# Kernel tuning notes

Hardware: AMD Instinct MI355X
Metric: run time of the kernel (lower is better)

Reference implementation:

```python
import jax, jax.numpy as jnp
import numpy as np

H = 16       # num_heads
D = 128      # head dim (TokenShift requires D in {16,32,64,128})
BASE = 10000.0


def _shift_linear(x, W, Ws):
    # ShiftLinear: linear -> (B,T,H,D), then token_shift mixing current token
    # with previous token using data-dependent per-head weights.
    B, T, _ = x.shape
    y = (x @ W.T).reshape(B, T, H, D)
    p = jax.nn.sigmoid(x @ Ws.T)                      # (B,T,H) prev-token weight
    y_prev = jnp.pad(y, ((0, 0), (1, 0), (0, 0), (0, 0)))[:, :T]  # shift right by 1
    return y * (1.0 - p)[..., None] + y_prev * p[..., None]


def _rope(q, k):
    # Non-interleaved half-rotation, signs exactly as in the torch source:
    # y1 = x1*cos + x2*sin ; y2 = -x1*sin + x2*cos
    T = q.shape[1]
    half = D // 2
    inv = 1.0 / (BASE ** (jnp.arange(0, D, 2, dtype=jnp.float32) / D))  # (half,)
    freqs = jnp.outer(jnp.arange(T, dtype=jnp.float32), inv)            # (T,half)
    cos = jnp.cos(freqs)[None, :, None, :]
    sin = jnp.sin(freqs)[None, :, None, :]
    def rot(x):
        x1, x2 = x[..., :half], x[..., half:]
        return jnp.concatenate([x1 * cos + x2 * sin, -x1 * sin + x2 * cos], axis=-1)
    return rot(q), rot(k)


def setup_inputs() -> dict:
    key = jax.random.key(0)
    ks = jax.random.split(key, 10)
    B, T, C = 2, 2048, 2048
    s = 0.02
    return {
        "x":   jax.random.normal(ks[0], (B, T, C), jnp.float32),
        "Wq":  s * jax.random.normal(ks[1], (C, C), jnp.float32),
        "Wsq": s * jax.random.normal(ks[2], (H, C), jnp.float32),
        "Wk":  s * jax.random.normal(ks[3], (C, C), jnp.float32),
        "Wsk": s * jax.random.normal(ks[4], (H, C), jnp.float32),
        "Wv":  s * jax.random.normal(ks[5], (C, C), jnp.float32),
        "Wsv": s * jax.random.normal(ks[6], (H, C), jnp.float32),
        "Wf":  s * jax.random.normal(ks[7], (H, C), jnp.float32),
        "bf":  s * jax.random.normal(ks[8], (H,), jnp.float32),
        "Wo":  s * jax.random.normal(ks[9], (C, C), jnp.float32),
    }


def reference(x, Wq, Wsq, Wk, Wsk, Wv, Wsv, Wf, bf, Wo):
    B, T, C = x.shape
    q = _shift_linear(x, Wq, Wsq)          # (B,T,H,D)
    k = _shift_linear(x, Wk, Wsk)
    v = _shift_linear(x, Wv, Wsv)
    q, k = _rope(q, k)

    # forget gate: log f_t per head, cumulative log-decay
    logf = jax.nn.log_sigmoid(x @ Wf.T + bf)       # (B,T,H)
    cum = jnp.cumsum(logf, axis=1).transpose(0, 2, 1)  # (B,H,T)

    s = jnp.einsum('bthd,bshd->bhts', q, k) / np.sqrt(D).astype(np.float32)
    # decay bias D_ij = sum_{l=j+1}^{i} log f_l = cum_i - cum_j
    s = s + cum[:, :, :, None] - cum[:, :, None, :]
    causal = jnp.tril(jnp.ones((T, T), dtype=bool))
    s = jnp.where(causal[None, None], s, -jnp.inf)
    p = jax.nn.softmax(s, axis=-1)                 # (B,H,T,T)

    o = jnp.einsum('bhts,bshd->bthd', p, v).reshape(B, T, C)
    return o @ Wo.T
```

## Files before the change

kernel.cpp:

```cpp
#include <hip/hip_runtime.h>
#include <math.h>


typedef __attribute__((ext_vector_type(8))) short  shortx8;
typedef __attribute__((ext_vector_type(4))) float  floatx4;

#define DEV __device__ __forceinline__

DEV unsigned short f2bf(float f) {
    unsigned int u = __builtin_bit_cast(unsigned int, f);
    u += 0x7FFFu + ((u >> 16) & 1u);
    return (unsigned short)(u >> 16);
}
DEV float bf2f(unsigned short s) {
    unsigned int u = ((unsigned int)s) << 16;
    return __builtin_bit_cast(float, u);
}
DEV void async16(void* lds, const void* g) {
    __builtin_amdgcn_global_load_lds(
        (const __attribute__((address_space(1))) unsigned int*)g,
        (__attribute__((address_space(3))) unsigned int*)lds, 16, 0, 0);
}

__global__ void cvt_bf16(const float* __restrict__ in, unsigned short* __restrict__ out, int n8) {
    int i = blockIdx.x * 256 + threadIdx.x;
    if (i >= n8) return;
    float4 u = ((const float4*)in)[2 * i];
    float4 v = ((const float4*)in)[2 * i + 1];
    shortx8 r;
    r[0] = (short)f2bf(u.x); r[1] = (short)f2bf(u.y); r[2] = (short)f2bf(u.z); r[3] = (short)f2bf(u.w);
    r[4] = (short)f2bf(v.x); r[5] = (short)f2bf(v.y); r[6] = (short)f2bf(v.z); r[7] = (short)f2bf(v.w);
    *(shortx8*)(out + (size_t)i * 8) = r;
}

__global__ void rope_tab(float2* __restrict__ tab, float* __restrict__ kmaxp) {
    int i = blockIdx.x * 256 + threadIdx.x;
    if (i < 32) kmaxp[i] = 0.f;
    int d = i & 63, t = i >> 6;
    float inv = exp2f(-(float)d * (13.287712379549449f / 64.f));
    float sv, cv;
    sincosf((float)t * inv, &sv, &cv);
    tab[i] = make_float2(cv, sv);
}

__global__ void build_wcat(const float* __restrict__ Wsq, const float* __restrict__ Wsk,
                           const float* __restrict__ Wsv, const float* __restrict__ Wf,
                           unsigned short* __restrict__ out) {
    int i = blockIdx.x * 256 + threadIdx.x;
    int c8 = i & 255;
    int row = i >> 8;
    const float* src = nullptr;
    if      (row < 16) src = Wsq + (size_t)row * 2048;
    else if (row < 32) src = Wsk + (size_t)(row - 16) * 2048;
    else if (row < 48) src = Wsv + (size_t)(row - 32) * 2048;
    else if (row < 64) src = Wf  + (size_t)(row - 48) * 2048;
    shortx8 r = (shortx8){0,0,0,0,0,0,0,0};
    if (src) {
#pragma unroll
        for (int q = 0; q < 8; ++q) r[q] = (short)f2bf(src[c8 * 8 + q]);
    }
    *(shortx8*)(out + (size_t)i * 8) = r;
}

template <typename OutT>
__global__ __launch_bounds__(256)
void gemm_bt(const unsigned short* __restrict__ A, const unsigned short* __restrict__ B,
             OutT* __restrict__ C, int M, int N, int K) {
    __shared__ __align__(16) unsigned short As[2][128 * 32];
    __shared__ __align__(16) unsigned short Bs[2][128 * 32];
    const int tid  = threadIdx.x;
    const int lane = tid & 63;
    const int w    = tid >> 6;
    const int nwg  = gridDim.x * gridDim.y;
    const int bid0 = blockIdx.y * gridDim.x + blockIdx.x;
    const int bids = (bid0 & 7) * (nwg >> 3) + (bid0 >> 3);
    const int m0   = (bids % gridDim.x) * 128;
    const int n0   = (bids / gridDim.x) * 128;
    const int wr   = (w >> 1) * 64;
    const int wc   = (w & 1) * 64;
    const int l15  = lane & 15, lg = lane >> 4;
    const int nk   = K >> 5;
    const int c0   = w * 64 + lane;

    floatx4 acc[4][4];
#pragma unroll
    for (int i = 0; i < 4; ++i)
#pragma unroll
        for (int j = 0; j < 4; ++j) acc[i][j] = (floatx4){0.f, 0.f, 0.f, 0.f};

#pragma unroll
    for (int t = 0; t < 2; ++t) {
        int c = t * 256 + c0;
        int row = c >> 2, seg = c & 3;
        async16(&As[0][(t * 256 + w * 64) * 8], A + (size_t)(m0 + row) * K + seg * 8);
        async16(&Bs[0][(t * 256 + w * 64) * 8], B + (size_t)(n0 + row) * K + seg * 8);
    }
    int cur = 0;
    for (int kt = 0; kt < nk; ++kt) {
        __syncthreads();
        if (kt + 1 < nk) {
#pragma unroll
            for (int t = 0; t < 2; ++t) {
                int c = t * 256 + c0;
                int row = c >> 2, seg = c & 3;
                async16(&As[cur ^ 1][(t * 256 + w * 64) * 8],
                        A + (size_t)(m0 + row) * K + (kt + 1) * 32 + seg * 8);
                async16(&Bs[cur ^ 1][(t * 256 + w * 64) * 8],
                        B + (size_t)(n0 + row) * K + (kt + 1) * 32 + seg * 8);
            }
        }
        shortx8 af[4], bfr[4];
#pragma unroll
        for (int i = 0; i < 4; ++i) {
            af[i]  = *(const shortx8*)&As[cur][(wr + i * 16 + l15) * 32 + 8 * lg];
            bfr[i] = *(const shortx8*)&Bs[cur][(wc + i * 16 + l15) * 32 + 8 * lg];
        }
#pragma unroll
        for (int i = 0; i < 4; ++i)
#pragma unroll
            for (int j = 0; j < 4; ++j)
                acc[i][j] = __builtin_amdgcn_mfma_f32_16x16x32_bf16(af[i], bfr[j], acc[i][j], 0, 0, 0);
        cur ^= 1;
    }
#pragma unroll
    for (int i = 0; i < 4; ++i)
#pragma unroll
        for (int j = 0; j < 4; ++j)
#pragma unroll
            for (int r = 0; r < 4; ++r) {
                int row = m0 + wr + i * 16 + 4 * lg + r;
                int col = n0 + wc + j * 16 + l15;
                float v = acc[i][j][r];
                if constexpr (sizeof(OutT) == 2) C[(size_t)row * N + col] = (OutT)f2bf(v);
                else                             C[(size_t)row * N + col] = v;
            }
}

__global__ void cumsum_logf(const float* __restrict__ glog, const float* __restrict__ bfv,
                            float* __restrict__ cum) {
    __shared__ float sums[256];
    const int bh = blockIdx.x, b = bh >> 4, h = bh & 15;
    const int tid = threadIdx.x;
    const float bias = bfv[h];
    float v[8];
    float s = 0.f;
#pragma unroll
    for (int i = 0; i < 8; ++i) {
        int t = tid * 8 + i;
        float z = glog[(size_t)(b * 2048 + t) * 128 + 48 + h] + bias;
        float lf = (z >= 0.f) ? -log1pf(__expf(-z)) : (z - log1pf(__expf(z)));
        s += lf;
        v[i] = s;
    }
    sums[tid] = s;
    __syncthreads();
    for (int off = 1; off < 256; off <<= 1) {
        float t = (tid >= off) ? sums[tid - off] : 0.f;
        __syncthreads();
        sums[tid] += t;
        __syncthreads();
    }
    float basep = sums[tid] - s;
#pragma unroll
    for (int i = 0; i < 8; ++i)
        cum[(size_t)bh * 2048 + tid * 8 + i] = basep + v[i];
}

template <bool ROPE>
__global__ void shift_rope(const unsigned short* __restrict__ Y, int ldY, int yoff,
                           const float* __restrict__ glog, int gcol,
                           const float4* __restrict__ tab4, float* __restrict__ kmaxp,
                           unsigned short* __restrict__ Out) {
    int gid = blockIdx.x * 256 + threadIdx.x;
    int j = gid & 7;
    int h = (gid >> 3) & 15;
    int t = (gid >> 7) & 2047;
    int b = gid >> 18;
    const unsigned short* yp = Y + (size_t)(b * 2048 + t) * ldY + yoff + h * 128;
    float z  = glog[(size_t)(b * 2048 + t) * 128 + gcol + h];
    float pg = 1.f / (1.f + __expf(-z));
    shortx8 a1 = *(const shortx8*)(yp + j * 8);
    shortx8 a2 = *(const shortx8*)(yp + 64 + j * 8);
    shortx8 b1 = (shortx8){0,0,0,0,0,0,0,0}, b2 = b1;
    if (t > 0) {
        b1 = *(const shortx8*)(yp - ldY + j * 8);
        b2 = *(const shortx8*)(yp - ldY + 64 + j * 8);
    }
    float c_[8], s_[8];
    if (ROPE && tab4) {
        const float4* tp = tab4 + (size_t)t * 32 + j * 4;
#pragma unroll
        for (int k = 0; k < 4; ++k) {
            float4 v4 = tp[k];
            c_[2 * k] = v4.x; s_[2 * k] = v4.y;
            c_[2 * k + 1] = v4.z; s_[2 * k + 1] = v4.w;
        }
    }
    shortx8 o1, o2;
    float n2 = 0.f;
    const float kf = 13.287712379549449f / 64.f;
#pragma unroll
    for (int i = 0; i < 8; ++i) {
        float m1 = bf2f((unsigned short)a1[i]) * (1.f - pg) + bf2f((unsigned short)b1[i]) * pg;
        float m2 = bf2f((unsigned short)a2[i]) * (1.f - pg) + bf2f((unsigned short)b2[i]) * pg;
        n2 += m1 * m1 + m2 * m2;
        float r1, r2;
        if (ROPE) {
            float sv, cv;
            if (tab4) { cv = c_[i]; sv = s_[i]; }
            else {
                int d = j * 8 + i;
                float inv = exp2f(-(float)d * kf);
                sincosf((float)t * inv, &sv, &cv);
            }
            r1 =  m1 * cv + m2 * sv;
            r2 = -m1 * sv + m2 * cv;
        } else { r1 = m1; r2 = m2; }
        o1[i] = (short)f2bf(r1);
        o2[i] = (short)f2bf(r2);
    }
    if (kmaxp) {
        n2 += __shfl_xor(n2, 1);
        n2 += __shfl_xor(n2, 2);
        n2 += __shfl_xor(n2, 4);
        if (j == 0)
            atomicMax((int*)(kmaxp + (b * 16 + h)), __float_as_int(n2));
    }
    unsigned short* op = Out + (size_t)((b * 16 + h) * 2048 + t) * 128;
    *(shortx8*)(op + j * 8)      = o1;
    *(shortx8*)(op + 64 + j * 8) = o2;
}

__global__ void transpose_v(const unsigned short* __restrict__ V, unsigned short* __restrict__ Vt) {
    __shared__ unsigned short tile[32][33];
    const int bh = blockIdx.z;
    const int t0 = blockIdx.x * 32, d0 = blockIdx.y * 32;
    const int tx = threadIdx.x, ty = threadIdx.y;
#pragma unroll
    for (int i = 0; i < 4; ++i) {
        int row = ty + i * 8;
        tile[row][tx] = V[(size_t)(bh * 2048 + t0 + row) * 128 + d0 + tx];
    }
    __syncthreads();
#pragma unroll
    for (int i = 0; i < 4; ++i) {
        int drow = ty + i * 8;
        Vt[(size_t)(bh * 128 + d0 + drow) * 2048 + t0 + tx] = tile[tx][drow];
    }
}

__global__ __launch_bounds__(512)
void flash_fwd(const unsigned short* __restrict__ Q, const unsigned short* __restrict__ Km,
               const unsigned short* __restrict__ Vt, const float* __restrict__ cum,
               const float* __restrict__ kmaxp, unsigned short* __restrict__ O) {
    __shared__ __align__(16) unsigned short Ks[3][32 * 128];
    __shared__ __align__(16) unsigned short Vs[3][64 * 64];
    __shared__ __align__(16) float          cumLds[2048];
    __shared__ __align__(16) unsigned short Plds[8][16][40];
    __shared__ int wmin[8];
    const int tid = threadIdx.x, lane = tid & 63, w = tid >> 6;
    const int l15 = lane & 15, lg = lane >> 4;
    const int bh = blockIdx.y, b = bh >> 4, h = bh & 15;
    const int qx = blockIdx.x;
    const int q0 = qx * 128;
    const int qr = q0 + w * 16;
    const size_t base = (size_t)bh * (2048 * 128);
    const float isd = 0.08838834764831845f;
    const int ntiles = 4 * qx + 4;
    const int myn0 = ((qr + 15) >> 5) + 1;
    const int myn = myn0 < ntiles ? myn0 : ntiles;

    const int ik = w * 64 + lane;
    const int kr = ik >> 4, kc = ik & 15;
    const unsigned short* ksrc = Km + base + (size_t)kr * 128 + ((kc ^ (kr & 7)) * 8);
    const int vr = ik >> 3, vc = ik & 7;
    const int vcc = vc ^ (vr & 7);
    const unsigned short* vsrc = Vt + (size_t)(bh * 128 + 2 * vr + (vcc >> 2)) * 2048 + (vcc & 3) * 8;

    const int kx = l15 & 7;
    const int vconst = ((l15 >> 1) * 64) + ((((l15 & 1) * 4 + lg) ^ ((l15 >> 1) & 7)) * 8);

    async16(&cumLds[ik * 4], cum + (size_t)bh * 2048 + ik * 4);
    shortx8 aq[4];
#pragma unroll
    for (int kk = 0; kk < 4; ++kk)
        aq[kk] = *(const shortx8*)(Q + base + (size_t)(qr + l15) * 128 + kk * 32 + 8 * lg);
    float kn2 = kmaxp ? kmaxp[bh] : 0.f;
    asm volatile("s_waitcnt vmcnt(0)" ::: "memory");
    __syncthreads();

    float cum_t[4];
#pragma unroll
    for (int r = 0; r < 4; ++r) cum_t[r] = cumLds[qr + 4 * lg + r];

    int wstart = 0;
    if (kmaxp) {
        float qp = 0.f;
#pragma unroll
        for (int kk = 0; kk < 4; ++kk)
#pragma unroll
            for (int i = 0; i < 8; ++i) {
                float v = bf2f((unsigned short)aq[kk][i]);
                qp += v * v;
            }
        qp += __shfl_xor(qp, 16);
        qp += __shfl_xor(qp, 32);
        float qn2 = qp;
        qn2 = fmaxf(qn2, __shfl_xor(qn2, 1));
        qn2 = fmaxf(qn2, __shfl_xor(qn2, 2));
        qn2 = fmaxf(qn2, __shfl_xor(qn2, 4));
        qn2 = fmaxf(qn2, __shfl_xor(qn2, 8));
        float qkb = sqrtf(qn2 * kn2) * isd;
        float thr = cumLds[qr] + 2.f * qkb + 30.f;
        int lo = 0, hi = myn - 1;
        while (lo < hi) {
            int mid = (lo + hi) >> 1;
            if (cumLds[32 * mid + 31] > thr) lo = mid + 1; else hi = mid;
        }
        wstart = lo;
    }
    if (lane == 0) wmin[w] = wstart;
    __syncthreads();
    int s0b = wmin[0];
#pragma unroll
    for (int i = 1; i < 8; ++i) s0b = min(s0b, wmin[i]);

    const int t2 = (s0b + 1 < ntiles) ? s0b + 1 : s0b;
    async16(&Ks[0][ik * 8], ksrc + (size_t)s0b * 32 * 128);
    async16(&Vs[0][ik * 8], vsrc + s0b * 32);
    async16(&Ks[1][ik * 8], ksrc + (size_t)t2 * 32 * 128);
    async16(&Vs[1][ik * 8], vsrc + t2 * 32);

    floatx4 oacc[8];
#pragma unroll
    for (int d = 0; d < 8; ++d) oacc[d] = (floatx4){0.f, 0.f, 0.f, 0.f};
    float m[4]  = {-1e30f, -1e30f, -1e30f, -1e30f};
    float ls[4] = {0.f, 0.f, 0.f, 0.f};

    int bc = 0, bi = 2;
    for (int kt = s0b; kt < ntiles; ++kt) {
        if (kt + 1 < ntiles) { asm volatile("s_waitcnt vmcnt(2)" ::: "memory"); }
        else                 { asm volatile("s_waitcnt vmcnt(0)" ::: "memory"); }
        __builtin_amdgcn_s_barrier();
        if (kt + 2 < ntiles) {
            async16(&Ks[bi][ik * 8], ksrc + (size_t)(kt + 2) * 32 * 128);
            async16(&Vs[bi][ik * 8], vsrc + (kt + 2) * 32);
        }
        if (kt >= wstart && kt < myn) {
            const int s0 = kt * 32;
            floatx4 sacc[2];
            sacc[0] = (floatx4){0.f, 0.f, 0.f, 0.f};
            sacc[1] = (floatx4){0.f, 0.f, 0.f, 0.f};
#pragma unroll
            for (int sf = 0; sf < 2; ++sf)
#pragma unroll
                for (int kk = 0; kk < 4; ++kk) {
                    shortx8 bk = *(const shortx8*)&Ks[bc][(sf * 16 + l15) * 128 + (((kk * 4 + lg) ^ kx) * 8)];
                    sacc[sf] = __builtin_amdgcn_mfma_f32_16x16x32_bf16(aq[kk], bk, sacc[sf], 0, 0, 0);
                }
            float cs[2];
#pragma unroll
            for (int sf = 0; sf < 2; ++sf) cs[sf] = cumLds[s0 + sf * 16 + l15];

            float p[2][4];
            float tmax[4] = {-1e30f, -1e30f, -1e30f, -1e30f};
            const bool maskt = (s0 + 31 > qr);
#pragma unroll
            for (int sf = 0; sf < 2; ++sf)
#pragma unroll
                for (int r = 0; r < 4; ++r) {
                    float sv = sacc[sf][r] * isd + cum_t[r] - cs[sf];
                    if (maskt) {
                        int trow = qr + 4 * lg + r;
                        int scol = s0 + sf * 16 + l15;
                        if (scol > trow) sv = -1e30f;
                    }
                    p[sf][r] = sv;
                    tmax[r] = fmaxf(tmax[r], sv);
                }
#pragma unroll
            for (int r = 0; r < 4; ++r) {
                tmax[r] = fmaxf(tmax[r], __shfl_xor(tmax[r], 1));
                tmax[r] = fmaxf(tmax[r], __shfl_xor(tmax[r], 2));
                tmax[r] = fmaxf(tmax[r], __shfl_xor(tmax[r], 4));
                tmax[r] = fmaxf(tmax[r], __shfl_xor(tmax[r], 8));
            }
            float g = tmax[0] - m[0];
            g = fmaxf(g, tmax[1] - m[1]);
            g = fmaxf(g, tmax[2] - m[2]);
            g = fmaxf(g, tmax[3] - m[3]);
            if (!__all(g <= 8.0f)) {
                float scl[4];
#pragma unroll
                for (int r = 0; r < 4; ++r) {
                    float mn = fmaxf(m[r], tmax[r]);
                    scl[r] = __expf(m[r] - mn);
                    m[r] = mn;
                    ls[r] *= scl[r];
                }
#pragma unroll
                for (int d = 0; d < 8; ++d)
#pragma unroll
                    for (int r = 0; r < 4; ++r) oacc[d][r] *= scl[r];
            }
            float rs[4] = {0.f, 0.f, 0.f, 0.f};
#pragma unroll
            for (int sf = 0; sf < 2; ++sf)
#pragma unroll
                for (int r = 0; r < 4; ++r) {
                    float e = __expf(p[sf][r] - m[r]);
                    p[sf][r] = e;
                    rs[r] += e;
                }
#pragma unroll
            for (int r = 0; r < 4; ++r) {
                rs[r] += __shfl_xor(rs[r], 1);
                rs[r] += __shfl_xor(rs[r], 2);
                rs[r] += __shfl_xor(rs[r], 4);
                rs[r] += __shfl_xor(rs[r], 8);
                ls[r] += rs[r];
            }
#pragma unroll
            for (int sf = 0; sf < 2; ++sf)
#pragma unroll
                for (int r = 0; r < 4; ++r)
                    Plds[w][4 * lg + r][sf * 16 + l15] = f2bf(p[sf][r]);
            shortx8 pa = *(const shortx8*)&Plds[w][l15][8 * lg];
#pragma unroll
            for (int d = 0; d < 8; ++d) {
                shortx8 bv = *(const shortx8*)&Vs[bc][d * 512 + vconst];
                oacc[d] = __builtin_amdgcn_mfma_f32_16x16x32_bf16(pa, bv, oacc[d], 0, 0, 0);
            }
        }
        bc = (bc == 2) ? 0 : bc + 1;
        bi = (bi == 2) ? 0 : bi + 1;
    }
#pragma unroll
    for (int r = 0; r < 4; ++r) {
        float inv = 1.f / ls[r];
        int trow = qr + 4 * lg + r;
        size_t ob = (size_t)(b * 2048 + trow) * 2048 + h * 128;
#pragma unroll
        for (int d = 0; d < 8; ++d)
            O[ob + d * 16 + l15] = f2bf(oacc[d][r] * inv);
    }
}

extern "C" void kernel_launch(void* const* d_in, const int* in_sizes, int n_in,
                              void* d_out, int out_size, void* d_ws, size_t ws_size,
                              hipStream_t stream) {
    const float* x   = (const float*)d_in[0];
    const float* Wq  = (const float*)d_in[1];
    const float* Wsq = (const float*)d_in[2];
    const float* Wk  = (const float*)d_in[3];
    const float* Wsk = (const float*)d_in[4];
    const float* Wv  = (const float*)d_in[5];
    const float* Wsv = (const float*)d_in[6];
    const float* Wf  = (const float*)d_in[7];
    const float* bfv = (const float*)d_in[8];
    const float* Wo  = (const float*)d_in[9];
    float* out = (float*)d_out;
    char* ws = (char*)d_ws;

    if (ws_size >= 146538880ull) {
        unsigned short* xb    = (unsigned short*)(ws + 0);
        unsigned short* Wb3   = (unsigned short*)(ws + 16777216);
        unsigned short* wcat  = (unsigned short*)(ws + 41943040);
        float*          glog  = (float*)(ws + 42467328);
        float*          cum   = (float*)(ws + 44564480);
        unsigned short* qbuf  = (unsigned short*)(ws + 44826624);
        unsigned short* kbuf  = (unsigned short*)(ws + 61603840);
        unsigned short* vbuf  = (unsigned short*)(ws + 78381056);
        float2*         tab   = (float2*)(ws + 95158272);
        float*          kmaxb = (float*)(ws + 96206848);
        unsigned short* ybuf3 = (unsigned short*)(ws + 96207232);
        unsigned short* vt    = ybuf3;

        cvt_bf16<<<4096, 256, 0, stream>>>(x, xb, 1048576);
        rope_tab<<<512, 256, 0, stream>>>(tab, kmaxb);
        build_wcat<<<128, 256, 0, stream>>>(Wsq, Wsk, Wsv, Wf, wcat);
        gemm_bt<float><<<dim3(32, 1), 256, 0, stream>>>(xb, wcat, glog, 4096, 128, 2048);
        cumsum_logf<<<32, 256, 0, stream>>>(glog, bfv, cum);

        cvt_bf16<<<2048, 256, 0, stream>>>(Wq, Wb3, 524288);
        cvt_bf16<<<2048, 256, 0, stream>>>(Wk, Wb3 + 4194304, 524288);
        cvt_bf16<<<2048, 256, 0, stream>>>(Wv, Wb3 + 8388608, 524288);
        gemm_bt<unsigned short><<<dim3(32, 48), 256, 0, stream>>>(xb, Wb3, ybuf3, 4096, 6144, 2048);

        shift_rope<true><<<2048, 256, 0, stream>>>(ybuf3, 6144, 0,    glog, 0,  (const float4*)tab, nullptr, qbuf);
        shift_rope<true><<<2048, 256, 0, stream>>>(ybuf3, 6144, 2048, glog, 16, (const float4*)tab, kmaxb,  kbuf);
        shift_rope<false><<<2048, 256, 0, stream>>>(ybuf3, 6144, 4096, glog, 32, nullptr, nullptr, vbuf);
        transpose_v<<<dim3(64, 4, 32), dim3(32, 8), 0, stream>>>(vbuf, vt);

        flash_fwd<<<dim3(16, 32), 512, 0, stream>>>(qbuf, kbuf, vt, cum, kmaxb, xb);

        cvt_bf16<<<2048, 256, 0, stream>>>(Wo, Wb3, 524288);
        gemm_bt<float><<<dim3(32, 16), 256, 0, stream>>>(xb, Wb3, out, 4096, 2048, 2048);
    } else {
        unsigned short* xb   = (unsigned short*)(ws + 0);
        unsigned short* Wb   = (unsigned short*)(ws + 16777216);
        unsigned short* wcat = (unsigned short*)(ws + 25165824);
        float*          glog = (float*)(ws + 25690112);
        float*          cum  = (float*)(ws + 27787264);
        unsigned short* ybuf = (unsigned short*)(ws + 28049408);
        unsigned short* qbuf = (unsigned short*)(ws + 44826624);
        unsigned short* kbuf = (unsigned short*)(ws + 61603840);
        unsigned short* vbuf = (unsigned short*)(ws + 78381056);
        unsigned short* vt   = (unsigned short*)(ws + 95158272);

        cvt_bf16<<<4096, 256, 0, stream>>>(x, xb, 1048576);
        build_wcat<<<128, 256, 0, stream>>>(Wsq, Wsk, Wsv, Wf, wcat);
        gemm_bt<float><<<dim3(32, 1), 256, 0, stream>>>(xb, wcat, glog, 4096, 128, 2048);
        cumsum_logf<<<32, 256, 0, stream>>>(glog, bfv, cum);

        cvt_bf16<<<2048, 256, 0, stream>>>(Wq, Wb, 524288);
        gemm_bt<unsigned short><<<dim3(32, 16), 256, 0, stream>>>(xb, Wb, ybuf, 4096, 2048, 2048);
        shift_rope<true><<<2048, 256, 0, stream>>>(ybuf, 2048, 0, glog, 0, nullptr, nullptr, qbuf);

        cvt_bf16<<<2048, 256, 0, stream>>>(Wk, Wb, 524288);
        gemm_bt<unsigned short><<<dim3(32, 16), 256, 0, stream>>>(xb, Wb, ybuf, 4096, 2048, 2048);
        shift_rope<true><<<2048, 256, 0, stream>>>(ybuf, 2048, 0, glog, 16, nullptr, nullptr, kbuf);

        cvt_bf16<<<2048, 256, 0, stream>>>(Wv, Wb, 524288);
        gemm_bt<unsigned short><<<dim3(32, 16), 256, 0, stream>>>(xb, Wb, ybuf, 4096, 2048, 2048);
        shift_rope<false><<<2048, 256, 0, stream>>>(ybuf, 2048, 0, glog, 32, nullptr, nullptr, vbuf);
        transpose_v<<<dim3(64, 4, 32), dim3(32, 8), 0, stream>>>(vbuf, vt);

        flash_fwd<<<dim3(16, 32), 512, 0, stream>>>(qbuf, kbuf, vt, cum, nullptr, ybuf);

        cvt_bf16<<<2048, 256, 0, stream>>>(Wo, Wb, 524288);
        gemm_bt<float><<<dim3(32, 16), 256, 0, stream>>>(ybuf, Wb, out, 4096, 2048, 2048);
    }
}
```

Measured before the change: 495.9 us.

## Add 256x256-tile GEMM with swizzled LDS and phased prefetch for QKV projection

Adds a new GEMM kernel using 256x256 output tiles, 512 threads, a 64-wide K step with XOR-swizzled LDS layout, double-buffered async global-to-LDS loads split across compute phases, and block-ID remapping for cache locality. The fused QKV projection (4096x6144x2048) switches to it. The larger tiles are meant to raise arithmetic intensity and cut global and LDS traffic per MFMA. In exchange it uses 128KB of LDS at one block per CU, so there are only 384 blocks and occupancy is low.

```diff
diff --git a/kernel.cpp b/kernel.cpp
--- a/kernel.cpp
+++ b/kernel.cpp
@@ -131,6 +131,117 @@
                 int row = m0 + wr + i * 16 + 4 * lg + r;
                 int col = n0 + wc + j * 16 + l15;
                 float v = acc[i][j][r];
+                if constexpr (sizeof(OutT) == 2) C[(size_t)row * N + col] = (OutT)f2bf(v);
+                else                             C[(size_t)row * N + col] = v;
+            }
+}
+
+template <typename OutT>
+__global__ __launch_bounds__(512, 1)
+void gemm_bt256(const unsigned short* __restrict__ A, const unsigned short* __restrict__ B,
+                OutT* __restrict__ C, int M, int N, int K) {
+    __shared__ __align__(16) unsigned short As[2][256 * 64];
+    __shared__ __align__(16) unsigned short Bs[2][256 * 64];
+    const int tid = threadIdx.x, lane = tid & 63, w = tid >> 6;
+    const int l15 = lane & 15, lg = lane >> 4;
+    const int nwg  = gridDim.x * gridDim.y;
+    const int bid0 = blockIdx.y * gridDim.x + blockIdx.x;
+    const int bids = (bid0 & 7) * (nwg >> 3) + (bid0 >> 3);
+    const int m0 = (bids % gridDim.x) * 256;
+    const int n0 = (bids / gridDim.x) * 256;
+    const int wr = (w >> 2) * 128;
+    const int wc = (w & 3) * 64;
+    const int nk = K >> 6;
+
+    const unsigned short* asrc[4];
+    const unsigned short* bsrc[4];
+    int cdst[4];
+#pragma unroll
+    for (int i = 0; i < 4; ++i) {
+        int c = tid + 512 * i;
+        int row = c >> 3, k8 = c & 7;
+        int k8s = k8 ^ (row & 7);
+        cdst[i] = c * 8;
+        asrc[i] = A + (size_t)(m0 + row) * K + k8s * 8;
+        bsrc[i] = B + (size_t)(n0 + row) * K + k8s * 8;
+    }
+    const int ch0 = (0 + lg) ^ (l15 & 7);
+    const int ch1 = (4 + lg) ^ (l15 & 7);
+
+    floatx4 acc[8][4];
+#pragma unroll
+    for (int i = 0; i < 8; ++i)
+#pragma unroll
+        for (int j = 0; j < 4; ++j) acc[i][j] = (floatx4){0.f, 0.f, 0.f, 0.f};
+
+#pragma unroll
+    for (int i = 0; i < 4; ++i) async16(&As[0][cdst[i]], asrc[i]);
+#pragma unroll
+    for (int i = 0; i < 4; ++i) async16(&Bs[0][cdst[i]], bsrc[i]);
+    asm volatile("s_waitcnt vmcnt(0)" ::: "memory");
+    __syncthreads();
+
+    for (int kt = 0; kt < nk; ++kt) {
+        const int p = kt & 1;
+        const unsigned short* Ap = &As[p][0];
+        const unsigned short* Bp = &Bs[p][0];
+        unsigned short* An = (unsigned short*)&As[p ^ 1][0];
+        unsigned short* Bn = (unsigned short*)&Bs[p ^ 1][0];
+        const bool more = (kt + 1 < nk);
+        const int koff = (kt + 1) * 64;
+#pragma unroll
+        for (int ph = 0; ph < 4; ++ph) {
+            const int mg = ph >> 1, ng = ph & 1;
+            shortx8 af[4][2], bfv[2][2];
+#pragma unroll
+            for (int mi = 0; mi < 4; ++mi) {
+                int row = wr + (mg * 4 + mi) * 16 + l15;
+                af[mi][0] = *(const shortx8*)&Ap[row * 64 + ch0 * 8];
+                af[mi][1] = *(const shortx8*)&Ap[row * 64 + ch1 * 8];
+            }
+#pragma unroll
+            for (int ni = 0; ni < 2; ++ni) {
+                int row = wc + (ng * 2 + ni) * 16 + l15;
+                bfv[ni][0] = *(const shortx8*)&Bp[row * 64 + ch0 * 8];
+                bfv[ni][1] = *(const shortx8*)&Bp[row * 64 + ch1 * 8];
+            }
+            if (more && ph == 0) {
+#pragma unroll
+                for (int i = 0; i < 4; ++i) async16(&An[cdst[i]], asrc[i] + koff);
+            }
+            if (more && ph == 1) {
+#pragma unroll
+                for (int i = 0; i < 4; ++i) async16(&Bn[cdst[i]], bsrc[i] + koff);
+            }
+            __builtin_amdgcn_s_barrier();
+            __builtin_amdgcn_s_setprio(1);
+#pragma unroll
+            for (int mi = 0; mi < 4; ++mi)
+#pragma unroll
+                for (int ni = 0; ni < 2; ++ni) {
+                    acc[mg * 4 + mi][ng * 2 + ni] = __builtin_amdgcn_mfma_f32_16x16x32_bf16(
+                        af[mi][0], bfv[ni][0], acc[mg * 4 + mi][ng * 2 + ni], 0, 0, 0);
+                    acc[mg * 4 + mi][ng * 2 + ni] = __builtin_amdgcn_mfma_f32_16x16x32_bf16(
+                        af[mi][1], bfv[ni][1], acc[mg * 4 + mi][ng * 2 + ni], 0, 0, 0);
+                }
+            __builtin_amdgcn_s_setprio(0);
+            if (ph < 3) {
+                __builtin_amdgcn_s_barrier();
+            } else {
+                asm volatile("s_waitcnt vmcnt(0)" ::: "memory");
+                __builtin_amdgcn_s_barrier();
+            }
+        }
+    }
+#pragma unroll
+    for (int mr = 0; mr < 8; ++mr)
+#pragma unroll
+        for (int nr = 0; nr < 4; ++nr)
+#pragma unroll
+            for (int r = 0; r < 4; ++r) {
+                int row = m0 + wr + mr * 16 + 4 * lg + r;
+                int col = n0 + wc + nr * 16 + l15;
+                float v = acc[mr][nr][r];
                 if constexpr (sizeof(OutT) == 2) C[(size_t)row * N + col] = (OutT)f2bf(v);
                 else                             C[(size_t)row * N + col] = v;
             }
@@ -485,7 +596,7 @@
         cvt_bf16<<<2048, 256, 0, stream>>>(Wq, Wb3, 524288);
         cvt_bf16<<<2048, 256, 0, stream>>>(Wk, Wb3 + 4194304, 524288);
         cvt_bf16<<<2048, 256, 0, stream>>>(Wv, Wb3 + 8388608, 524288);
-        gemm_bt<unsigned short><<<dim3(32, 48), 256, 0, stream>>>(xb, Wb3, ybuf3, 4096, 6144, 2048);
+        gemm_bt256<unsigned short><<<dim3(16, 24), 512, 0, stream>>>(xb, Wb3, ybuf3, 4096, 6144, 2048);
 
         shift_rope<true><<<2048, 256, 0, stream>>>(ybuf3, 6144, 0,    glog, 0,  (const float4*)tab, nullptr, qbuf);
         shift_rope<true><<<2048, 256, 0, stream>>>(ybuf3, 6144, 2048, glog, 16, (const float4*)tab, kmaxb,  kbuf);
```

After: 509.6 us. 1.03x slower.
